# Kernel tuning notes

Measured on AMD Instinct MI355X. Metric: run time of the kernel, lower is better.

## Reference

```python
import jax, jax.numpy as jnp
import numpy as np

N, L = 8192, 4096
AFWD = 0.999
EPS = 1e-05


def setup_inputs() -> dict:
    key = jax.random.key(0)
    x = jax.random.normal(key, (N, L), dtype=jnp.float32)
    mu0 = jnp.zeros((L,), dtype=jnp.float32)   # buffer m, init 0
    var0 = jnp.ones((L,), dtype=jnp.float32)   # buffer var, init 1
    return {"x": x, "mu0": mu0, "var0": var0}


def reference(x, mu0, var0):
    """Online Normalization forward (training mode): sequential per-sample
    EMA mean/variance recurrence over the batch dim.
      y_t   = (x_t - mu_{t-1}) / sqrt(var_{t-1} + eps)
      var_t = afwd*var_{t-1} + afwd*(1-afwd)*(x_t - mu_{t-1})^2
      mu_t  = afwd*mu_{t-1} + (1-afwd)*x_t
    """
    def step(carry, xt):
        mu, var = carry                      # [L], [L]
        scale = jnp.sqrt(var + EPS)          # [L]
        d = xt - mu                          # [L]
        out = d / scale
        var = AFWD * var + AFWD * (1.0 - AFWD) * d * d
        mu = mu + (1.0 - AFWD) * d           # == afwd*mu + (1-afwd)*x
        return (mu, var), out

    (_, _), out = jax.lax.scan(step, (mu0, var0), x)  # out: [N, L]
    return out
```

## Files before the change

kernel.cpp:

```cpp
#include <hip/hip_runtime.h>
#include <math.h>

static constexpr float AFWD = 0.999f;
static constexpr float EPS  = 1e-5f;

typedef float vfloat4 __attribute__((ext_vector_type(4)));

__global__ __launch_bounds__(256) void onlnorm_pass1(
    const float* __restrict__ x, float* __restrict__ Sv,
    float* __restrict__ T0v, float* __restrict__ Ev, int n, int L)
{
    const int chunk = blockIdx.y;
    const int col = (blockIdx.x * blockDim.x + threadIdx.x) * 4;
    if (col >= L) return;
    const float a = AFWD, b = 1.0f - AFWD, ab = AFWD * (1.0f - AFWD);
    const float* xp = x + (size_t)chunk * (size_t)n * L + col;

    float m0=0.f,m1=0.f,m2=0.f,m3=0.f;
    float t0=0.f,t1=0.f,t2=0.f,t3=0.f;
    float e0=0.f,e1=0.f,e2=0.f,e3=0.f;

    constexpr int PF = 8;

#define P1_STEP(xv)                                                   \
    do { float d;                                                     \
        d = (xv).x - m0; e0 += d; t0 = a*t0 + ab*d*d; m0 += b*d;      \
        d = (xv).y - m1; e1 += d; t1 = a*t1 + ab*d*d; m1 += b*d;      \
        d = (xv).z - m2; e2 += d; t2 = a*t2 + ab*d*d; m2 += b*d;      \
        d = (xv).w - m3; e3 += d; t3 = a*t3 + ab*d*d; m3 += b*d;      \
    } while (0)

    if ((n % PF) == 0 && n >= 2 * PF) {
        float4 buf[PF];
        #pragma unroll
        for (int j = 0; j < PF; ++j)
            buf[j] = *reinterpret_cast<const float4*>(xp + (size_t)j * L);
        for (int i0 = 0; i0 + PF < n; i0 += PF) {
            #pragma unroll
            for (int j = 0; j < PF; ++j) {
                const float4 xv = buf[j];
                buf[j] = *reinterpret_cast<const float4*>(xp + (size_t)(i0 + PF + j) * L);
                P1_STEP(xv);
            }
        }
        #pragma unroll
        for (int j = 0; j < PF; ++j) { const float4 xv = buf[j]; P1_STEP(xv); }
    } else {
        for (int i = 0; i < n; ++i) {
            const float4 xv = *reinterpret_cast<const float4*>(xp + (size_t)i * L);
            P1_STEP(xv);
        }
    }
#undef P1_STEP

    const size_t base = (size_t)chunk * L + col;
    *reinterpret_cast<float4*>(Sv  + base) = make_float4(m0,m1,m2,m3);
    *reinterpret_cast<float4*>(T0v + base) = make_float4(t0,t1,t2,t3);
    *reinterpret_cast<float4*>(Ev  + base) = make_float4(e0,e1,e2,e3);
}

__global__ __launch_bounds__(128) void onlnorm_pass2(
    const float* __restrict__ Sv, const float* __restrict__ T0v,
    const float* __restrict__ Ev, const float* __restrict__ mu0,
    const float* __restrict__ var0, float* __restrict__ muin,
    float* __restrict__ varin, int C, int L, float A, float B, float W)
{
    const int col = blockIdx.x * blockDim.x + threadIdx.x;
    if (col >= L) return;
    float mu = mu0[col], var = var0[col];
    constexpr int BATCH = 32;
    float sb[BATCH], tb[BATCH], eb[BATCH];
    int c0 = 0;
    for (; c0 + BATCH <= C; c0 += BATCH) {
        #pragma unroll
        for (int j = 0; j < BATCH; ++j) {
            const size_t idx = (size_t)(c0 + j) * L + col;
            sb[j] = Sv[idx]; tb[j] = T0v[idx]; eb[j] = Ev[idx];
        }
        #pragma unroll
        for (int j = 0; j < BATCH; ++j) {
            const size_t idx = (size_t)(c0 + j) * L + col;
            muin[idx]  = mu;
            varin[idx] = var;
            var = A*var + tb[j] - 2.0f*B*mu*eb[j] + W*mu*mu;
            mu  = A*mu + sb[j];
        }
    }
    for (; c0 < C; ++c0) {
        const size_t idx = (size_t)c0 * L + col;
        muin[idx] = mu; varin[idx] = var;
        const float s = Sv[idx], t = T0v[idx], e = Ev[idx];
        var = A*var + t - 2.0f*B*mu*e + W*mu*mu;
        mu  = A*mu + s;
    }
}

__global__ __launch_bounds__(256) void onlnorm_pass3(
    const float* __restrict__ x, const float* __restrict__ muin,
    const float* __restrict__ varin, float* __restrict__ out, int n, int L)
{
    const int chunk = blockIdx.y;
    const int col = (blockIdx.x * blockDim.x + threadIdx.x) * 4;
    if (col >= L) return;
    const float a = AFWD, b = 1.0f - AFWD, ab = AFWD * (1.0f - AFWD);
    const size_t cbase = (size_t)chunk * L + col;
    const float4 muv  = *reinterpret_cast<const float4*>(muin  + cbase);
    const float4 varv = *reinterpret_cast<const float4*>(varin + cbase);
    float m0=muv.x, m1=muv.y, m2=muv.z, m3=muv.w;
    float v0=varv.x, v1=varv.y, v2=varv.z, v3=varv.w;
    const float* xp = x   + (size_t)chunk * (size_t)n * L + col;
    float*       op = out + (size_t)chunk * (size_t)n * L + col;

    constexpr int PF = 8;

#define P3_STEP(xv, row)                                                        \
    do { vfloat4 ov; float d;                                                   \
        d = (xv).x - m0; ov.x = d * rsqrtf(v0 + EPS); v0 = a*v0 + ab*d*d; m0 += b*d; \
        d = (xv).y - m1; ov.y = d * rsqrtf(v1 + EPS); v1 = a*v1 + ab*d*d; m1 += b*d; \
        d = (xv).z - m2; ov.z = d * rsqrtf(v2 + EPS); v2 = a*v2 + ab*d*d; m2 += b*d; \
        d = (xv).w - m3; ov.w = d * rsqrtf(v3 + EPS); v3 = a*v3 + ab*d*d; m3 += b*d; \
        __builtin_nontemporal_store(ov, reinterpret_cast<vfloat4*>(op + (size_t)(row) * L)); \
    } while (0)

    if ((n % PF) == 0 && n >= 2 * PF) {
        float4 buf[PF];
        #pragma unroll
        for (int j = 0; j < PF; ++j)
            buf[j] = *reinterpret_cast<const float4*>(xp + (size_t)j * L);
        for (int i0 = 0; i0 + PF < n; i0 += PF) {
            #pragma unroll
            for (int j = 0; j < PF; ++j) {
                const float4 xv = buf[j];
                buf[j] = *reinterpret_cast<const float4*>(xp + (size_t)(i0 + PF + j) * L);
                P3_STEP(xv, i0 + j);
            }
        }
        const int ie = n - PF;
        #pragma unroll
        for (int j = 0; j < PF; ++j) { const float4 xv = buf[j]; P3_STEP(xv, ie + j); }
    } else {
        for (int i = 0; i < n; ++i) {
            const float4 xv = *reinterpret_cast<const float4*>(xp + (size_t)i * L);
            P3_STEP(xv, i);
        }
    }
#undef P3_STEP
}

extern "C" void kernel_launch(void* const* d_in, const int* in_sizes, int n_in,
                              void* d_out, int out_size, void* d_ws, size_t ws_size,
                              hipStream_t stream) {
    const float* x    = (const float*)d_in[0];
    const float* mu0  = (const float*)d_in[1];
    const float* var0 = (const float*)d_in[2];
    float* out = (float*)d_out;

    const int L = in_sizes[1];
    const int N = in_sizes[0] / L;

    int C = 256;
    while (C > 1 && ((size_t)5 * (size_t)C * L * sizeof(float) > ws_size ||
                     (N % C) != 0 || ((N / C) % 8) != 0))
        C >>= 1;
    const int n = N / C;

    float* Sv    = (float*)d_ws;
    float* T0v   = Sv    + (size_t)C * L;
    float* Ev    = T0v   + (size_t)C * L;
    float* muin  = Ev    + (size_t)C * L;
    float* varin = muin  + (size_t)C * L;

    const double a  = (double)AFWD;
    const double An = pow(a, (double)n);
    const float A = (float)An;
    const float B = (float)(An * (1.0 - a));
    const float W = (float)(An * (1.0 - An));

    const dim3 blk(256);
    const dim3 g1((L / 4 + 255) / 256, C);

    onlnorm_pass1<<<g1, blk, 0, stream>>>(x, Sv, T0v, Ev, n, L);
    onlnorm_pass2<<<dim3((L + 127) / 128), dim3(128), 0, stream>>>(
        Sv, T0v, Ev, mu0, var0, muin, varin, C, L, A, B, W);
    onlnorm_pass3<<<g1, blk, 0, stream>>>(x, muin, varin, out, n, L);
}
```

Measured before the change: 82.23 us.

## Fuse three passes into one cooperative kernel with grid-wide syncs

Merges the chunk-summary pass, the cross-chunk scan and the output pass into one cooperative kernel separated by two grid syncs. The grid is limited to 512 blocks, so C drops to 128 and each chunk holds more rows. This removes two kernel launches and their gaps. In exchange it pays for grid barriers, leaves most blocks idle during the scan phase, and gives less parallelism per pass than the old C=256 layout. The old three-kernel path stays as a fallback and drops its divisibility-by-8 check on n.

```diff
diff --git a/kernel.cpp b/kernel.cpp
--- a/kernel.cpp
+++ b/kernel.cpp
@@ -1,10 +1,138 @@
 #include <hip/hip_runtime.h>
+#include <hip/hip_cooperative_groups.h>
 #include <math.h>
+
+namespace cg = cooperative_groups;
 
 static constexpr float AFWD = 0.999f;
 static constexpr float EPS  = 1e-5f;
 
 typedef float vfloat4 __attribute__((ext_vector_type(4)));
+
+__global__ __launch_bounds__(256, 2) void onlnorm_fused(
+    const float* __restrict__ x,
+    const float* __restrict__ mu0, const float* __restrict__ var0,
+    float* __restrict__ out,
+    float* __restrict__ Sv, float* __restrict__ T0v, float* __restrict__ Ev,
+    float* __restrict__ muin, float* __restrict__ varin,
+    int n, int L, int C, float A, float B, float W)
+{
+    const float a = AFWD, b = 1.0f - AFWD, ab = AFWD * (1.0f - AFWD);
+    const int chunk = blockIdx.y;
+    const int col = (blockIdx.x * blockDim.x + threadIdx.x) * 4;
+    const bool active = (col < L);
+    constexpr int PF = 8;
+
+    if (active) {
+        const float* xp = x + (size_t)chunk * (size_t)n * L + col;
+        float m0=0.f,m1=0.f,m2=0.f,m3=0.f;
+        float t0=0.f,t1=0.f,t2=0.f,t3=0.f;
+        float e0=0.f,e1=0.f,e2=0.f,e3=0.f;
+
+#define P1_STEP(xv)                                                   \
+    do { float d;                                                     \
+        d = (xv).x - m0; e0 += d; t0 = a*t0 + ab*d*d; m0 += b*d;      \
+        d = (xv).y - m1; e1 += d; t1 = a*t1 + ab*d*d; m1 += b*d;      \
+        d = (xv).z - m2; e2 += d; t2 = a*t2 + ab*d*d; m2 += b*d;      \
+        d = (xv).w - m3; e3 += d; t3 = a*t3 + ab*d*d; m3 += b*d;      \
+    } while (0)
+
+        float4 buf[PF];
+        #pragma unroll
+        for (int j = 0; j < PF; ++j)
+            buf[j] = *reinterpret_cast<const float4*>(xp + (size_t)j * L);
+        for (int i0 = 0; i0 + PF < n; i0 += PF) {
+            #pragma unroll
+            for (int j = 0; j < PF; ++j) {
+                const float4 xv = buf[j];
+                buf[j] = *reinterpret_cast<const float4*>(xp + (size_t)(i0 + PF + j) * L);
+                P1_STEP(xv);
+            }
+        }
+        #pragma unroll
+        for (int j = 0; j < PF; ++j) { const float4 xv = buf[j]; P1_STEP(xv); }
+#undef P1_STEP
+
+        const size_t base = (size_t)chunk * L + col;
+        *reinterpret_cast<float4*>(Sv  + base) = make_float4(m0,m1,m2,m3);
+        *reinterpret_cast<float4*>(T0v + base) = make_float4(t0,t1,t2,t3);
+        *reinterpret_cast<float4*>(Ev  + base) = make_float4(e0,e1,e2,e3);
+    }
+    cg::this_grid().sync();
+
+    {
+        const int bid = blockIdx.y * gridDim.x + blockIdx.x;
+        const int nscan = (L + 255) / 256;
+        if (bid < nscan) {
+            const int scol = bid * 256 + (int)threadIdx.x;
+            if (scol < L) {
+                float mu = mu0[scol], var = var0[scol];
+                constexpr int BATCH = 16;
+                float sb[BATCH], tb[BATCH], eb[BATCH];
+                int c0 = 0;
+                for (; c0 + BATCH <= C; c0 += BATCH) {
+                    #pragma unroll
+                    for (int j = 0; j < BATCH; ++j) {
+                        const size_t idx = (size_t)(c0 + j) * L + scol;
+                        sb[j] = Sv[idx]; tb[j] = T0v[idx]; eb[j] = Ev[idx];
+                    }
+                    #pragma unroll
+                    for (int j = 0; j < BATCH; ++j) {
+                        const size_t idx = (size_t)(c0 + j) * L + scol;
+                        muin[idx]  = mu;
+                        varin[idx] = var;
+                        var = A*var + tb[j] - 2.0f*B*mu*eb[j] + W*mu*mu;
+                        mu  = A*mu + sb[j];
+                    }
+                }
+                for (; c0 < C; ++c0) {
+                    const size_t idx = (size_t)c0 * L + scol;
+                    muin[idx] = mu; varin[idx] = var;
+                    const float s = Sv[idx], t = T0v[idx], e = Ev[idx];
+                    var = A*var + t - 2.0f*B*mu*e + W*mu*mu;
+                    mu  = A*mu + s;
+                }
+            }
+        }
+    }
+    cg::this_grid().sync();
+
+    if (active) {
+        const size_t cbase = (size_t)chunk * L + col;
+        const float4 muv  = *reinterpret_cast<const float4*>(muin  + cbase);
+        const float4 varv = *reinterpret_cast<const float4*>(varin + cbase);
+        float m0=muv.x, m1=muv.y, m2=muv.z, m3=muv.w;
+        float v0=varv.x, v1=varv.y, v2=varv.z, v3=varv.w;
+        const float* xp = x   + (size_t)chunk * (size_t)n * L + col;
+        float*       op = out + (size_t)chunk * (size_t)n * L + col;
+
+#define P3_STEP(xv, row)                                                        \
+    do { vfloat4 ov; float d;                                                   \
+        d = (xv).x - m0; ov.x = d * rsqrtf(v0 + EPS); v0 = a*v0 + ab*d*d; m0 += b*d; \
+        d = (xv).y - m1; ov.y = d * rsqrtf(v1 + EPS); v1 = a*v1 + ab*d*d; m1 += b*d; \
+        d = (xv).z - m2; ov.z = d * rsqrtf(v2 + EPS); v2 = a*v2 + ab*d*d; m2 += b*d; \
+        d = (xv).w - m3; ov.w = d * rsqrtf(v3 + EPS); v3 = a*v3 + ab*d*d; m3 += b*d; \
+        __builtin_nontemporal_store(ov, reinterpret_cast<vfloat4*>(op + (size_t)(row) * L)); \
+    } while (0)
+
+        float4 buf[PF];
+        #pragma unroll
+        for (int j = 0; j < PF; ++j)
+            buf[j] = *reinterpret_cast<const float4*>(xp + (size_t)j * L);
+        for (int i0 = 0; i0 + PF < n; i0 += PF) {
+            #pragma unroll
+            for (int j = 0; j < PF; ++j) {
+                const float4 xv = buf[j];
+                buf[j] = *reinterpret_cast<const float4*>(xp + (size_t)(i0 + PF + j) * L);
+                P3_STEP(xv, i0 + j);
+            }
+        }
+        const int ie = n - PF;
+        #pragma unroll
+        for (int j = 0; j < PF; ++j) { const float4 xv = buf[j]; P3_STEP(xv, ie + j); }
+#undef P3_STEP
+    }
+}
 
 __global__ __launch_bounds__(256) void onlnorm_pass1(
     const float* __restrict__ x, float* __restrict__ Sv,
@@ -15,13 +143,10 @@
     if (col >= L) return;
     const float a = AFWD, b = 1.0f - AFWD, ab = AFWD * (1.0f - AFWD);
     const float* xp = x + (size_t)chunk * (size_t)n * L + col;
-
     float m0=0.f,m1=0.f,m2=0.f,m3=0.f;
     float t0=0.f,t1=0.f,t2=0.f,t3=0.f;
     float e0=0.f,e1=0.f,e2=0.f,e3=0.f;
-
     constexpr int PF = 8;
-
 #define P1_STEP(xv)                                                   \
     do { float d;                                                     \
         d = (xv).x - m0; e0 += d; t0 = a*t0 + ab*d*d; m0 += b*d;      \
@@ -29,7 +154,6 @@
         d = (xv).z - m2; e2 += d; t2 = a*t2 + ab*d*d; m2 += b*d;      \
         d = (xv).w - m3; e3 += d; t3 = a*t3 + ab*d*d; m3 += b*d;      \
     } while (0)
-
     if ((n % PF) == 0 && n >= 2 * PF) {
         float4 buf[PF];
         #pragma unroll
@@ -52,7 +176,6 @@
         }
     }
 #undef P1_STEP
-
     const size_t base = (size_t)chunk * L + col;
     *reinterpret_cast<float4*>(Sv  + base) = make_float4(m0,m1,m2,m3);
     *reinterpret_cast<float4*>(T0v + base) = make_float4(t0,t1,t2,t3);
@@ -110,9 +233,7 @@
     float v0=varv.x, v1=varv.y, v2=varv.z, v3=varv.w;
     const float* xp = x   + (size_t)chunk * (size_t)n * L + col;
     float*       op = out + (size_t)chunk * (size_t)n * L + col;
-
     constexpr int PF = 8;
-
 #define P3_STEP(xv, row)                                                        \
     do { vfloat4 ov; float d;                                                   \
         d = (xv).x - m0; ov.x = d * rsqrtf(v0 + EPS); v0 = a*v0 + ab*d*d; m0 += b*d; \
@@ -121,7 +242,6 @@
         d = (xv).w - m3; ov.w = d * rsqrtf(v3 + EPS); v3 = a*v3 + ab*d*d; m3 += b*d; \
         __builtin_nontemporal_store(ov, reinterpret_cast<vfloat4*>(op + (size_t)(row) * L)); \
     } while (0)
-
     if ((n % PF) == 0 && n >= 2 * PF) {
         float4 buf[PF];
         #pragma unroll
@@ -158,9 +278,46 @@
     const int L = in_sizes[1];
     const int N = in_sizes[0] / L;
 
+    const int gx = (L / 4 + 255) / 256;
+
+    {
+        int C = 128;
+        while (C > 1 && (gx * C > 512 ||
+                         (size_t)5 * (size_t)C * L * sizeof(float) > ws_size ||
+                         (N % C) != 0 || ((N / C) % 16) != 0))
+            C >>= 1;
+        const int n = N / C;
+
+        if ((n % 16) == 0 && gx * C <= 512 &&
+            (size_t)5 * (size_t)C * L * sizeof(float) <= ws_size) {
+            float* Sv    = (float*)d_ws;
+            float* T0v   = Sv    + (size_t)C * L;
+            float* Ev    = T0v   + (size_t)C * L;
+            float* muin  = Ev    + (size_t)C * L;
+            float* varin = muin  + (size_t)C * L;
+
+            const double a  = (double)AFWD;
+            const double An = pow(a, (double)n);
+            float A = (float)An;
+            float B = (float)(An * (1.0 - a));
+            float W = (float)(An * (1.0 - An));
+
+            dim3 grid(gx, C), block(256);
+            int n_ = n, L_ = L, C_ = C;
+            void* args[] = {
+                (void*)&x, (void*)&mu0, (void*)&var0, (void*)&out,
+                (void*)&Sv, (void*)&T0v, (void*)&Ev, (void*)&muin, (void*)&varin,
+                (void*)&n_, (void*)&L_, (void*)&C_, (void*)&A, (void*)&B, (void*)&W
+            };
+            hipError_t err = hipLaunchCooperativeKernel((void*)onlnorm_fused,
+                                                        grid, block, args, 0u, stream);
+            if (err == hipSuccess) return;
+        }
+    }
+
     int C = 256;
     while (C > 1 && ((size_t)5 * (size_t)C * L * sizeof(float) > ws_size ||
-                     (N % C) != 0 || ((N / C) % 8) != 0))
+                     (N % C) != 0))
         C >>= 1;
     const int n = N / C;
 
@@ -178,7 +335,6 @@
 
     const dim3 blk(256);
     const dim3 g1((L / 4 + 255) / 256, C);
-
     onlnorm_pass1<<<g1, blk, 0, stream>>>(x, Sv, T0v, Ev, n, L);
     onlnorm_pass2<<<dim3((L + 127) / 128), dim3(128), 0, stream>>>(
         Sv, T0v, Ev, mu0, var0, muin, varin, C, L, A, B, W);
```

Result: slower. 199.7 us (+142.9%).

## Fuse chunk-summary and scan passes via atomic counter spin-wait in one launch

Applied to the files above, without the earlier changes.

Merges the per-chunk summary kernel and the cross-chunk scan kernel into a single launch. Extra trailing blocks spin on a global atomic counter until every producer block has published its partials, then run the column scan. This removes one kernel launch and its inter-kernel gap. It adds a hipMemsetAsync, relies on the scan blocks being dispatched after the producers so the spin does not deadlock, and the scan blocks occupy CU slots while they wait. The scan batch size also drops from 32 to 16.

```diff
diff --git a/kernel.cpp b/kernel.cpp
--- a/kernel.cpp
+++ b/kernel.cpp
@@ -6,21 +6,28 @@
 
 typedef float vfloat4 __attribute__((ext_vector_type(4)));
 
-__global__ __launch_bounds__(256) void onlnorm_pass1(
-    const float* __restrict__ x, float* __restrict__ Sv,
-    float* __restrict__ T0v, float* __restrict__ Ev, int n, int L)
+__global__ __launch_bounds__(256) void onlnorm_pass1f(
+    const float* __restrict__ x,
+    float* __restrict__ Sv, float* __restrict__ T0v, float* __restrict__ Ev,
+    const float* __restrict__ mu0, const float* __restrict__ var0,
+    float* __restrict__ muin, float* __restrict__ varin,
+    int* __restrict__ counter,
+    int n, int L, int C, int gx, float A, float B, float W)
 {
-    const int chunk = blockIdx.y;
-    const int col = (blockIdx.x * blockDim.x + threadIdx.x) * 4;
-    if (col >= L) return;
     const float a = AFWD, b = 1.0f - AFWD, ab = AFWD * (1.0f - AFWD);
-    const float* xp = x + (size_t)chunk * (size_t)n * L + col;
-
-    float m0=0.f,m1=0.f,m2=0.f,m3=0.f;
-    float t0=0.f,t1=0.f,t2=0.f,t3=0.f;
-    float e0=0.f,e1=0.f,e2=0.f,e3=0.f;
-
-    constexpr int PF = 8;
+    const int bid = blockIdx.x;
+    const int nprod = gx * C;
+
+    if (bid < nprod) {
+        const int chunk = bid / gx;
+        const int g = bid % gx;
+        const int col = (g * 256 + (int)threadIdx.x) * 4;
+        if (col < L) {
+            const float* xp = x + (size_t)chunk * (size_t)n * L + col;
+            float m0=0.f,m1=0.f,m2=0.f,m3=0.f;
+            float t0=0.f,t1=0.f,t2=0.f,t3=0.f;
+            float e0=0.f,e1=0.f,e2=0.f,e3=0.f;
+            constexpr int PF = 8;
 
 #define P1_STEP(xv)                                                   \
     do { float d;                                                     \
@@ -30,68 +37,76 @@
         d = (xv).w - m3; e3 += d; t3 = a*t3 + ab*d*d; m3 += b*d;      \
     } while (0)
 
-    if ((n % PF) == 0 && n >= 2 * PF) {
-        float4 buf[PF];
-        #pragma unroll
-        for (int j = 0; j < PF; ++j)
-            buf[j] = *reinterpret_cast<const float4*>(xp + (size_t)j * L);
-        for (int i0 = 0; i0 + PF < n; i0 += PF) {
-            #pragma unroll
-            for (int j = 0; j < PF; ++j) {
-                const float4 xv = buf[j];
-                buf[j] = *reinterpret_cast<const float4*>(xp + (size_t)(i0 + PF + j) * L);
-                P1_STEP(xv);
-            }
-        }
-        #pragma unroll
-        for (int j = 0; j < PF; ++j) { const float4 xv = buf[j]; P1_STEP(xv); }
+            if ((n % PF) == 0 && n >= 2 * PF) {
+                float4 buf[PF];
+                #pragma unroll
+                for (int j = 0; j < PF; ++j)
+                    buf[j] = *reinterpret_cast<const float4*>(xp + (size_t)j * L);
+                for (int i0 = 0; i0 + PF < n; i0 += PF) {
+                    #pragma unroll
+                    for (int j = 0; j < PF; ++j) {
+                        const float4 xv = buf[j];
+                        buf[j] = *reinterpret_cast<const float4*>(xp + (size_t)(i0 + PF + j) * L);
+                        P1_STEP(xv);
+                    }
+                }
+                #pragma unroll
+                for (int j = 0; j < PF; ++j) { const float4 xv = buf[j]; P1_STEP(xv); }
+            } else {
+                for (int i = 0; i < n; ++i) {
+                    const float4 xv = *reinterpret_cast<const float4*>(xp + (size_t)i * L);
+                    P1_STEP(xv);
+                }
+            }
+#undef P1_STEP
+
+            const size_t base = (size_t)chunk * L + col;
+            *reinterpret_cast<float4*>(Sv  + base) = make_float4(m0,m1,m2,m3);
+            *reinterpret_cast<float4*>(T0v + base) = make_float4(t0,t1,t2,t3);
+            *reinterpret_cast<float4*>(Ev  + base) = make_float4(e0,e1,e2,e3);
+        }
+        __threadfence();
+        __syncthreads();
+        if (threadIdx.x == 0)
+            __hip_atomic_fetch_add(counter, 1, __ATOMIC_RELEASE,
+                                   __HIP_MEMORY_SCOPE_AGENT);
     } else {
-        for (int i = 0; i < n; ++i) {
-            const float4 xv = *reinterpret_cast<const float4*>(xp + (size_t)i * L);
-            P1_STEP(xv);
-        }
-    }
-#undef P1_STEP
-
-    const size_t base = (size_t)chunk * L + col;
-    *reinterpret_cast<float4*>(Sv  + base) = make_float4(m0,m1,m2,m3);
-    *reinterpret_cast<float4*>(T0v + base) = make_float4(t0,t1,t2,t3);
-    *reinterpret_cast<float4*>(Ev  + base) = make_float4(e0,e1,e2,e3);
-}
-
-__global__ __launch_bounds__(128) void onlnorm_pass2(
-    const float* __restrict__ Sv, const float* __restrict__ T0v,
-    const float* __restrict__ Ev, const float* __restrict__ mu0,
-    const float* __restrict__ var0, float* __restrict__ muin,
-    float* __restrict__ varin, int C, int L, float A, float B, float W)
-{
-    const int col = blockIdx.x * blockDim.x + threadIdx.x;
-    if (col >= L) return;
-    float mu = mu0[col], var = var0[col];
-    constexpr int BATCH = 32;
-    float sb[BATCH], tb[BATCH], eb[BATCH];
-    int c0 = 0;
-    for (; c0 + BATCH <= C; c0 += BATCH) {
-        #pragma unroll
-        for (int j = 0; j < BATCH; ++j) {
-            const size_t idx = (size_t)(c0 + j) * L + col;
-            sb[j] = Sv[idx]; tb[j] = T0v[idx]; eb[j] = Ev[idx];
-        }
-        #pragma unroll
-        for (int j = 0; j < BATCH; ++j) {
-            const size_t idx = (size_t)(c0 + j) * L + col;
-            muin[idx]  = mu;
-            varin[idx] = var;
-            var = A*var + tb[j] - 2.0f*B*mu*eb[j] + W*mu*mu;
-            mu  = A*mu + sb[j];
-        }
-    }
-    for (; c0 < C; ++c0) {
-        const size_t idx = (size_t)c0 * L + col;
-        muin[idx] = mu; varin[idx] = var;
-        const float s = Sv[idx], t = T0v[idx], e = Ev[idx];
-        var = A*var + t - 2.0f*B*mu*e + W*mu*mu;
-        mu  = A*mu + s;
+        if (threadIdx.x == 0) {
+            while (__hip_atomic_load(counter, __ATOMIC_ACQUIRE,
+                                     __HIP_MEMORY_SCOPE_AGENT) < nprod)
+                __builtin_amdgcn_s_sleep(32);
+        }
+        __syncthreads();
+
+        const int scol = (bid - nprod) * 256 + (int)threadIdx.x;
+        if (scol < L) {
+            float mu = mu0[scol], var = var0[scol];
+            constexpr int BATCH = 16;
+            float sb[BATCH], tb[BATCH], eb[BATCH];
+            int c0 = 0;
+            for (; c0 + BATCH <= C; c0 += BATCH) {
+                #pragma unroll
+                for (int j = 0; j < BATCH; ++j) {
+                    const size_t idx = (size_t)(c0 + j) * L + scol;
+                    sb[j] = Sv[idx]; tb[j] = T0v[idx]; eb[j] = Ev[idx];
+                }
+                #pragma unroll
+                for (int j = 0; j < BATCH; ++j) {
+                    const size_t idx = (size_t)(c0 + j) * L + scol;
+                    muin[idx]  = mu;
+                    varin[idx] = var;
+                    var = A*var + tb[j] - 2.0f*B*mu*eb[j] + W*mu*mu;
+                    mu  = A*mu + sb[j];
+                }
+            }
+            for (; c0 < C; ++c0) {
+                const size_t idx = (size_t)c0 * L + scol;
+                muin[idx] = mu; varin[idx] = var;
+                const float s = Sv[idx], t = T0v[idx], e = Ev[idx];
+                var = A*var + t - 2.0f*B*mu*e + W*mu*mu;
+                mu  = A*mu + s;
+            }
+        }
     }
 }
 
@@ -110,7 +125,6 @@
     float v0=varv.x, v1=varv.y, v2=varv.z, v3=varv.w;
     const float* xp = x   + (size_t)chunk * (size_t)n * L + col;
     float*       op = out + (size_t)chunk * (size_t)n * L + col;
-
     constexpr int PF = 8;
 
 #define P3_STEP(xv, row)                                                        \
@@ -158,17 +172,20 @@
     const int L = in_sizes[1];
     const int N = in_sizes[0] / L;
 
+    const int gx = (L / 4 + 255) / 256;
+
     int C = 256;
-    while (C > 1 && ((size_t)5 * (size_t)C * L * sizeof(float) > ws_size ||
-                     (N % C) != 0 || ((N / C) % 8) != 0))
+    while (C > 1 && (256 + (size_t)5 * (size_t)C * L * sizeof(float) > ws_size ||
+                     (N % C) != 0))
         C >>= 1;
     const int n = N / C;
 
-    float* Sv    = (float*)d_ws;
-    float* T0v   = Sv    + (size_t)C * L;
-    float* Ev    = T0v   + (size_t)C * L;
-    float* muin  = Ev    + (size_t)C * L;
-    float* varin = muin  + (size_t)C * L;
+    int*   counter = (int*)d_ws;
+    float* Sv      = (float*)((char*)d_ws + 256);
+    float* T0v     = Sv    + (size_t)C * L;
+    float* Ev      = T0v   + (size_t)C * L;
+    float* muin    = Ev    + (size_t)C * L;
+    float* varin   = muin  + (size_t)C * L;
 
     const double a  = (double)AFWD;
     const double An = pow(a, (double)n);
@@ -176,11 +193,13 @@
     const float B = (float)(An * (1.0 - a));
     const float W = (float)(An * (1.0 - An));
 
-    const dim3 blk(256);
-    const dim3 g1((L / 4 + 255) / 256, C);
-
-    onlnorm_pass1<<<g1, blk, 0, stream>>>(x, Sv, T0v, Ev, n, L);
-    onlnorm_pass2<<<dim3((L + 127) / 128), dim3(128), 0, stream>>>(
-        Sv, T0v, Ev, mu0, var0, muin, varin, C, L, A, B, W);
-    onlnorm_pass3<<<g1, blk, 0, stream>>>(x, muin, varin, out, n, L);
+    const int nprod = gx * C;
+    const int nscan = (L + 255) / 256;
+
+    hipMemsetAsync(counter, 0, sizeof(int), stream);
+    onlnorm_pass1f<<<dim3(nprod + nscan), dim3(256), 0, stream>>>(
+        x, Sv, T0v, Ev, mu0, var0, muin, varin, counter,
+        n, L, C, gx, A, B, W);
+    onlnorm_pass3<<<dim3(gx, C), dim3(256), 0, stream>>>(
+        x, muin, varin, out, n, L);
 }
```

New measurement: 245.4 us. +198.4%, slower.
